# Optimization experiments

Measured on AMD Instinct MI355X. Metric: run time of the kernel, lower is better.

Reference implementation:

```python
import jax, jax.numpy as jnp
import numpy as np

B, N = 64, 4096          # trees per batch, leaves per complete binary tree
V, S = 21, 50            # amino-acid vocab, grammar-symbol vocab
E, H = 64, 128           # embed_dim, hidden_dim


def setup_inputs() -> dict:
    key = jax.random.key(0)
    ks = jax.random.split(key, 16)

    def lin_w(k, din, dout):
        return (jax.random.normal(k, (dout, din), jnp.float32) / np.sqrt(din)).astype(jnp.float32)

    tokens = jax.random.randint(ks[0], (B, N), 0, V, dtype=jnp.int32)
    symbols = jax.random.randint(ks[1], (B, N - 1), 0, S, dtype=jnp.int32)

    emb = jax.random.normal(ks[2], (V, E), jnp.float32) * 0.02
    emb = emb.at[0].set(0.0)  # padding_idx=0
    sym_emb = jax.random.normal(ks[3], (S, E), jnp.float32) * 0.02

    return {
        "tokens": tokens, "symbols": symbols,
        "emb": emb, "sym_emb": sym_emb,
        "Wp": lin_w(ks[4], E, H), "bp": jnp.zeros((H,), jnp.float32),
        "Wi": lin_w(ks[5], H, H), "bi": jnp.zeros((H,), jnp.float32),
        "Ui": lin_w(ks[6], H, H),
        "Wf": lin_w(ks[7], H, H), "bf": jnp.zeros((H,), jnp.float32),
        "Uf": lin_w(ks[8], H, H),
        "Wo": lin_w(ks[9], H, H), "bo": jnp.zeros((H,), jnp.float32),
        "Uo": lin_w(ks[10], H, H),
        "Wu": lin_w(ks[11], H, H), "bu": jnp.zeros((H,), jnp.float32),
        "Uu": lin_w(ks[12], H, H),
        "Wout": lin_w(ks[13], H, H), "bout": jnp.zeros((H,), jnp.float32),
    }


def _encode(tokens, symbols, emb, sym_emb, Wp, bp, Wi, bi, Ui, Wf, bf, Uf,
            Wo, bo, Uo, Wu, bu, Uu, Wout, bout):
    emb = emb.at[0].set(0.0)  # padding row contributes nothing (and gets no grad)

    # Leaf nodes: amino-acid embedding -> input_proj, no children.
    x = emb[tokens] @ Wp.T + bp                      # [B, N, H]
    i = jax.nn.sigmoid(x @ Wi.T + bi)
    o = jax.nn.sigmoid(x @ Wo.T + bo)
    u = jnp.tanh(x @ Wu.T + bu)
    c = i * u                                        # [B, N, H]
    h = o * jnp.tanh(c)

    # Bottom-up over levels of the complete binary tree (Child-Sum Tree-LSTM).
    off, n = 0, N
    while n > 1:
        m = n // 2
        xs = sym_emb[symbols[:, off:off + m]] @ Wp.T + bp   # [B, m, H]
        hl, hr = h[:, 0::2], h[:, 1::2]
        cl, cr = c[:, 0::2], c[:, 1::2]
        ht = hl + hr                                         # h_tilde = sum_j h_j
        gi = jax.nn.sigmoid(xs @ Wi.T + bi + ht @ Ui.T)
        go = jax.nn.sigmoid(xs @ Wo.T + bo + ht @ Uo.T)
        gu = jnp.tanh(xs @ Wu.T + bu + ht @ Uu.T)
        fx = xs @ Wf.T + bf
        fl = jax.nn.sigmoid(fx + hl @ Uf.T)                  # per-child forget gates
        fr = jax.nn.sigmoid(fx + hr @ Uf.T)
        c = gi * gu + fl * cl + fr * cr
        h = go * jnp.tanh(c)
        off += m
        n = m

    root_h = h[:, 0]                                         # [B, H]
    return root_h @ Wout.T + bout                            # output_proj


def reference(tokens, symbols, emb, sym_emb, Wp, bp, Wi, bi, Ui, Wf, bf, Uf,
              Wo, bo, Uo, Wu, bu, Uu, Wout, bout):
    return _encode(tokens, symbols, emb, sym_emb, Wp, bp, Wi, bi, Ui, Wf, bf,
                   Uf, Wo, bo, Uo, Wu, bu, Uu, Wout, bout)
```

## Files before the change

### kernel.cpp

```cpp
#include <hip/hip_runtime.h>
#include <hip/hip_bf16.h>

typedef __attribute__((ext_vector_type(8))) short short8;
typedef __attribute__((ext_vector_type(4))) float f32x4;

static constexpr int B_ = 64;
static constexpr int N_ = 4096;
static constexpr int V_ = 21;
static constexpr int S_ = 50;
static constexpr int E_ = 64;
static constexpr int H_ = 128;
static constexpr int NPAIR = V_ * V_;
static constexpr int NTAB = NPAIR * S_;

__device__ __forceinline__ float rcp_(float x) { return __builtin_amdgcn_rcpf(x); }
__device__ __forceinline__ float sigm(float x) { return rcp_(1.0f + __expf(-x)); }
__device__ __forceinline__ float tanh_(float x) {
  float a = fabsf(x);
  float e = __expf(-2.0f * a);
  float t = (1.0f - e) * rcp_(1.0f + e);
  return x < 0.0f ? -t : t;
}
__device__ __forceinline__ unsigned short f2bf(float f) {
  __hip_bfloat16 b = __float2bfloat16(f);
  return *reinterpret_cast<unsigned short*>(&b);
}
__device__ __forceinline__ float bf2f(unsigned short u) {
  return __uint_as_float(((unsigned int)u) << 16);
}

__global__ void k_pre(const float* __restrict__ emb, const float* __restrict__ sym_emb,
                      const float* __restrict__ Wp, const float* __restrict__ bp,
                      const float* __restrict__ Wi, const float* __restrict__ bi, const float* __restrict__ Ui,
                      const float* __restrict__ Wf, const float* __restrict__ bf, const float* __restrict__ Uf,
                      const float* __restrict__ Wo, const float* __restrict__ bo, const float* __restrict__ Uo,
                      const float* __restrict__ Wu, const float* __restrict__ bu, const float* __restrict__ Uu,
                      unsigned short* __restrict__ Wfrag, float* __restrict__ Wt,
                      unsigned short* __restrict__ leaf_h8, float* __restrict__ leaf_c,
                      float* __restrict__ symx) {
  int blk = blockIdx.x, t = threadIdx.x;
  if (blk < 32) {
    int idx = blk * 256 + t;
    int L = idx & 63;
    int K = (idx >> 6) & 3;
    int T = idx >> 8;
    int n = 16 * T + (L & 15);
    int k0 = 32 * K + ((L >> 4) << 3);
    int g = n >> 7, o = n & 127;
    const float* U = (g == 0) ? Ui : (g == 1) ? Uo : (g == 2) ? Uu : Uf;
    unsigned short out[8];
    #pragma unroll
    for (int j = 0; j < 8; ++j) out[j] = f2bf(U[o * 128 + k0 + j]);
    *(int4*)(Wfrag + (size_t)idx * 8) = *(int4*)out;
  } else if (blk < 32 + V_) {
    int v = blk - 32;
    __shared__ float x[128];
    if (t < 128) {
      float acc = bp[t];
      if (v != 0) {
        for (int e = 0; e < E_; ++e) acc = fmaf(emb[v * E_ + e], Wp[t * E_ + e], acc);
      }
      x[t] = acc;
    }
    __syncthreads();
    if (t < 128) {
      float zi = bi[t], zo = bo[t], zu = bu[t];
      for (int k = 0; k < H_; ++k) {
        float xv = x[k];
        zi = fmaf(xv, Wi[t * H_ + k], zi);
        zo = fmaf(xv, Wo[t * H_ + k], zo);
        zu = fmaf(xv, Wu[t * H_ + k], zu);
      }
      float gi = sigm(zi), go = sigm(zo), gu = tanh_(zu);
      float c = gi * gu;
      leaf_c[v * H_ + t] = c;
      leaf_h8[v * H_ + t] = f2bf(go * tanh_(c));
    }
  } else if (blk < 32 + V_ + S_) {
    int s = blk - 32 - V_;
    __shared__ float x[128];
    if (t < 128) {
      float acc = bp[t];
      for (int e = 0; e < E_; ++e) acc = fmaf(sym_emb[s * E_ + e], Wp[t * E_ + e], acc);
      x[t] = acc;
    }
    __syncthreads();
    if (t < 128) {
      float zi = bi[t], zo = bo[t], zu = bu[t], zf = bf[t];
      for (int k = 0; k < H_; ++k) {
        float xv = x[k];
        zi = fmaf(xv, Wi[t * H_ + k], zi);
        zo = fmaf(xv, Wo[t * H_ + k], zo);
        zu = fmaf(xv, Wu[t * H_ + k], zu);
        zf = fmaf(xv, Wf[t * H_ + k], zf);
      }
      size_t base = (size_t)s * 4 * H_;
      symx[base + 0 * H_ + t] = zi;
      symx[base + 1 * H_ + t] = zo;
      symx[base + 2 * H_ + t] = zu;
      symx[base + 3 * H_ + t] = zf;
    }
  } else {
    int base = ((blk - 103) * 256 + t) * 8;
    int k = base >> 9;
    int col = base & 511;
    int gg = col >> 7, o0 = col & 127;
    const float* U = (gg == 0) ? Ui : (gg == 1) ? Uo : (gg == 2) ? Uu : Uf;
    float v[8];
    #pragma unroll
    for (int j = 0; j < 8; ++j) v[j] = U[(o0 + j) * 128 + k];
    *(float4*)(Wt + base) = *(float4*)v;
    *(float4*)(Wt + base + 4) = *(float4*)(v + 4);
  }
}

__global__ void k_tabA(const unsigned short* __restrict__ leaf_h8, const float* __restrict__ Wt,
                       float* __restrict__ za) {
  int p = blockIdx.x, t = threadIdx.x;
  int tl = p / V_, tr = p % V_;
  __shared__ float hl[128], hr[128];
  hl[t] = bf2f(leaf_h8[tl * H_ + t]);
  hr[t] = bf2f(leaf_h8[tr * H_ + t]);
  __syncthreads();
  float zi = 0.f, zo = 0.f, zu = 0.f, pfl = 0.f, pfr = 0.f;
  for (int k = 0; k < H_; ++k) {
    float l = hl[k], r = hr[k], ht = l + r;
    const float* wr = Wt + k * 512;
    zi = fmaf(ht, wr[t], zi);
    zo = fmaf(ht, wr[128 + t], zo);
    zu = fmaf(ht, wr[256 + t], zu);
    float wf = wr[384 + t];
    pfl = fmaf(l, wf, pfl);
    pfr = fmaf(r, wf, pfr);
  }
  float* z = za + (size_t)p * 640;
  z[t] = zi; z[128 + t] = zo; z[256 + t] = zu; z[384 + t] = pfl; z[512 + t] = pfr;
}

__global__ void k_tabB(const float* __restrict__ za, const float* __restrict__ symx,
                       const float* __restrict__ leaf_c,
                       const int* __restrict__ tokens, const int* __restrict__ symbols,
                       unsigned short* __restrict__ tab_h8, float* __restrict__ tab_c,
                       int* __restrict__ idx1) {
  int blk = blockIdx.x, t = threadIdx.x;
  if (blk < NTAB / 2) {
    int row = blk * 2 + (t >> 7);
    int u = t & 127;
    int p = row / S_, s = row - p * S_;
    int tl = p / V_, tr = p - tl * V_;
    const float* z = za + (size_t)p * 640;
    const float* sx = symx + (size_t)s * 512;
    float gi = sigm(sx[u] + z[u]);
    float go = sigm(sx[128 + u] + z[128 + u]);
    float gu = tanh_(sx[256 + u] + z[256 + u]);
    float fx = sx[384 + u];
    float fl = sigm(fx + z[384 + u]);
    float fr = sigm(fx + z[512 + u]);
    float cv = fmaf(gi, gu, fmaf(fl, leaf_c[tl * H_ + u], fr * leaf_c[tr * H_ + u]));
    tab_c[(size_t)row * H_ + u] = cv;
    tab_h8[(size_t)row * H_ + u] = f2bf(go * tanh_(cv));
  } else {
    int g = (blk - NTAB / 2) * 256 + t;
    int b = g >> 11, j = g & 2047;
    idx1[g] = (tokens[b * N_ + 2 * j] * V_ + tokens[b * N_ + 2 * j + 1]) * S_ + symbols[b * (N_ - 1) + j];
  }
}

template <bool GATHER>
__global__ void __launch_bounds__(512, 2) k_level(
    const unsigned short* __restrict__ Wfrag, const float* __restrict__ symx,
    const int* __restrict__ symbols, int sym_off, int lgm,
    const unsigned short* __restrict__ h_prev8, const float* __restrict__ c_prev,
    const int* __restrict__ gidx,
    const unsigned short* __restrict__ gh8, const float* __restrict__ gc,
    unsigned short* __restrict__ h_out8, float* __restrict__ c_out) {
  __shared__ __align__(16) unsigned short Asm[32][136];
  int t = threadIdx.x;
  int w = t >> 6, L = t & 63, q = L >> 4, cL = L & 15;
  int g0 = blockIdx.x * 16;

  {
    int row = t >> 4, co = (t & 15) * 8;
    const unsigned short* src = GATHER
        ? gh8 + (size_t)gidx[2 * g0 + row] * H_ + co
        : h_prev8 + (size_t)(2 * g0 + row) * H_ + co;
    *(int4*)&Asm[row][co] = *(const int4*)src;
  }
  __syncthreads();

  f32x4 acc[2][4];
  #pragma unroll
  for (int r = 0; r < 2; ++r)
    #pragma unroll
    for (int g = 0; g < 4; ++g) acc[r][g] = (f32x4){0.f, 0.f, 0.f, 0.f};

  const short8* wf = (const short8*)Wfrag;
  #pragma unroll
  for (int K = 0; K < 4; ++K) {
    short8 bfr[4];
    #pragma unroll
    for (int g = 0; g < 4; ++g) bfr[g] = wf[(size_t)((w + 8 * g) * 4 + K) * 64 + L];
    short8 a0 = *(const short8*)&Asm[cL][K * 32 + q * 8];
    short8 a1 = *(const short8*)&Asm[16 + cL][K * 32 + q * 8];
    #pragma unroll
    for (int g = 0; g < 4; ++g) {
      acc[0][g] = __builtin_amdgcn_mfma_f32_16x16x32_bf16(a0, bfr[g], acc[0][g], 0, 0, 0);
      acc[1][g] = __builtin_amdgcn_mfma_f32_16x16x32_bf16(a1, bfr[g], acc[1][g], 0, 0, 0);
    }
  }

  int cc = 16 * w + cL;
  int mmask = (1 << lgm) - 1;
  #pragma unroll
  for (int r = 0; r < 2; ++r) {
    #pragma unroll
    for (int nd = 0; nd < 2; ++nd) {
      int n = 8 * r + 2 * q + nd;
      int g = g0 + n;
      int bb = g >> lgm, jj = g & mmask;
      int s = symbols[bb * (N_ - 1) + sym_off + jj];
      const float* sx = symx + (size_t)s * 512;
      const float* clp;
      const float* crp;
      if (GATHER) {
        clp = gc + (size_t)gidx[2 * g] * H_;
        crp = gc + (size_t)gidx[2 * g + 1] * H_;
      } else {
        clp = c_prev + (size_t)(2 * g) * H_;
        crp = c_prev + (size_t)(2 * g + 1) * H_;
      }
      float i_p = acc[r][0][2 * nd] + acc[r][0][2 * nd + 1];
      float o_p = acc[r][1][2 * nd] + acc[r][1][2 * nd + 1];
      float u_p = acc[r][2][2 * nd] + acc[r][2][2 * nd + 1];
      float fl_p = acc[r][3][2 * nd];
      float fr_p = acc[r][3][2 * nd + 1];
      float gi = sigm(sx[cc] + i_p);
      float go = sigm(sx[128 + cc] + o_p);
      float gu = tanh_(sx[256 + cc] + u_p);
      float fx = sx[384 + cc];
      float fl = sigm(fx + fl_p);
      float fr = sigm(fx + fr_p);
      float cv = fmaf(gi, gu, fmaf(fl, clp[cc], fr * crp[cc]));
      c_out[(size_t)g * H_ + cc] = cv;
      h_out8[(size_t)g * H_ + cc] = f2bf(go * tanh_(cv));
    }
  }
}

__global__ void __launch_bounds__(512, 1) k_deep(
    const unsigned short* __restrict__ Wfrag, const float* __restrict__ symx,
    const int* __restrict__ symbols,
    const unsigned short* __restrict__ in_h8, const float* __restrict__ in_c,
    float* __restrict__ out_root) {
  __shared__ __align__(16) unsigned short Asm[64][136];
  __shared__ float Csm0[64][128];
  __shared__ float Csm1[32][128];
  int t = threadIdx.x;
  int w = t >> 6, L = t & 63, q = L >> 4, cL = L & 15;
  int b = blockIdx.x;

  #pragma unroll
  for (int i = 0; i < 2; ++i) {
    int fid = t + 512 * i;
    int row = fid >> 4, co = (fid & 15) * 8;
    *(int4*)&Asm[row][co] = *(const int4*)(in_h8 + (size_t)(b * 64 + row) * H_ + co);
  }
  #pragma unroll
  for (int i = 0; i < 4; ++i) {
    int fid = t + 512 * i;
    int row = fid >> 5, c4 = (fid & 31) << 2;
    *(float4*)&Csm0[row][c4] = *(const float4*)(in_c + (size_t)(b * 64 + row) * H_ + c4);
  }
  __syncthreads();

  const short8* wf = (const short8*)Wfrag;
  int cc = 16 * w + cL;
  int R = 64;
  #pragma unroll
  for (int lev = 0; lev < 6; ++lev) {
    const int l = 7 + lev;
    const int nodes = R >> 1;
    const int jb = b * (N_ - 1) + (N_ - (N_ >> (l - 1)));
    const int nchunk = (R + 31) >> 5;
    for (int c = 0; c < nchunk; ++c) {
      f32x4 acc[2][4];
      #pragma unroll
      for (int r = 0; r < 2; ++r)
        #pragma unroll
        for (int g = 0; g < 4; ++g) acc[r][g] = (f32x4){0.f, 0.f, 0.f, 0.f};
      #pragma unroll
      for (int K = 0; K < 4; ++K) {
        short8 bfr[4];
        #pragma unroll
        for (int g = 0; g < 4; ++g) bfr[g] = wf[(size_t)((w + 8 * g) * 4 + K) * 64 + L];
        short8 a0 = *(const short8*)&Asm[32 * c + cL][K * 32 + q * 8];
        short8 a1 = *(const short8*)&Asm[32 * c + 16 + cL][K * 32 + q * 8];
        #pragma unroll
        for (int g = 0; g < 4; ++g) {
          acc[0][g] = __builtin_amdgcn_mfma_f32_16x16x32_bf16(a0, bfr[g], acc[0][g], 0, 0, 0);
          acc[1][g] = __builtin_amdgcn_mfma_f32_16x16x32_bf16(a1, bfr[g], acc[1][g], 0, 0, 0);
        }
      }
      __syncthreads();
      const float* crd = (l & 1) ? &Csm0[0][0] : &Csm1[0][0];
      float* cwr = (l & 1) ? &Csm1[0][0] : &Csm0[0][0];
      #pragma unroll
      for (int r = 0; r < 2; ++r) {
        #pragma unroll
        for (int nd = 0; nd < 2; ++nd) {
          int n = 16 * c + 8 * r + 2 * q + nd;
          if (n < nodes) {
            int s = symbols[jb + n];
            const float* sx = symx + (size_t)s * 512;
            float i_p = acc[r][0][2 * nd] + acc[r][0][2 * nd + 1];
            float o_p = acc[r][1][2 * nd] + acc[r][1][2 * nd + 1];
            float u_p = acc[r][2][2 * nd] + acc[r][2][2 * nd + 1];
            float fl_p = acc[r][3][2 * nd];
            float fr_p = acc[r][3][2 * nd + 1];
            float gi = sigm(sx[cc] + i_p);
            float go = sigm(sx[128 + cc] + o_p);
            float gu = tanh_(sx[256 + cc] + u_p);
            float fx = sx[384 + cc];
            float fl = sigm(fx + fl_p);
            float fr = sigm(fx + fr_p);
            float cv = fmaf(gi, gu, fmaf(fl, crd[(size_t)(2 * n) * 128 + cc],
                                         fr * crd[(size_t)(2 * n + 1) * 128 + cc]));
            float hv = go * tanh_(cv);
            if (lev == 5) {
              out_root[(size_t)b * H_ + cc] = hv;
            } else {
              cwr[(size_t)n * 128 + cc] = cv;
              Asm[n][cc] = f2bf(hv);
            }
          }
        }
      }
      __syncthreads();
    }
    R >>= 1;
  }
}

__global__ void k_out(const float* __restrict__ hroot, const float* __restrict__ Wout,
                      const float* __restrict__ bout, float* __restrict__ out) {
  int b = blockIdx.x, o = threadIdx.x;
  __shared__ float hr[128];
  hr[o] = hroot[(size_t)b * H_ + o];
  __syncthreads();
  float acc = bout[o];
  for (int k = 0; k < H_; ++k) acc = fmaf(hr[k], Wout[o * H_ + k], acc);
  out[(size_t)b * H_ + o] = acc;
}

extern "C" void kernel_launch(void* const* d_in, const int* in_sizes, int n_in,
                              void* d_out, int out_size, void* d_ws, size_t ws_size,
                              hipStream_t stream) {
  const int* tokens    = (const int*)d_in[0];
  const int* symbols   = (const int*)d_in[1];
  const float* emb     = (const float*)d_in[2];
  const float* sym_emb = (const float*)d_in[3];
  const float* Wp  = (const float*)d_in[4];
  const float* bp  = (const float*)d_in[5];
  const float* Wi  = (const float*)d_in[6];
  const float* bi  = (const float*)d_in[7];
  const float* Ui  = (const float*)d_in[8];
  const float* Wf  = (const float*)d_in[9];
  const float* bf  = (const float*)d_in[10];
  const float* Uf  = (const float*)d_in[11];
  const float* Wo  = (const float*)d_in[12];
  const float* bo  = (const float*)d_in[13];
  const float* Uo  = (const float*)d_in[14];
  const float* Wu  = (const float*)d_in[15];
  const float* bu  = (const float*)d_in[16];
  const float* Uu  = (const float*)d_in[17];
  const float* Wout= (const float*)d_in[18];
  const float* bout= (const float*)d_in[19];

  char* ws = (char*)d_ws;
  unsigned short* Wfrag   = (unsigned short*)(ws);
  float*          Wt      = (float*)(ws + 131072);
  unsigned short* leaf_h8 = (unsigned short*)(ws + 393216);
  float*          leaf_c  = (float*)(ws + 398592);
  float*          symx    = (float*)(ws + 409344);
  float*          za      = (float*)(ws + 511744);
  unsigned short* tab_h8  = (unsigned short*)(ws + 1640704);
  float*          tab_c   = (float*)(ws + 7285504UL);
  int*            idx1    = (int*)(ws + 18575104UL);
  float*          hroot   = (float*)(ws + 19099392UL);
  unsigned short* A_h8    = (unsigned short*)(ws + 19132160UL);
  float*          A_c     = (float*)(ws + 35909376UL);
  unsigned short* B_h8    = (unsigned short*)(ws + 69463808UL);
  float*          B_c     = (float*)(ws + 77852416UL);

  k_pre<<<135, 256, 0, stream>>>(emb, sym_emb, Wp, bp,
      Wi, bi, Ui, Wf, bf, Uf, Wo, bo, Uo, Wu, bu, Uu,
      Wfrag, Wt, leaf_h8, leaf_c, symx);
  k_tabA<<<NPAIR, 128, 0, stream>>>(leaf_h8, Wt, za);
  k_tabB<<<NTAB / 2 + 512, 256, 0, stream>>>(za, symx, leaf_c, tokens, symbols,
      tab_h8, tab_c, idx1);

  unsigned short* prev_h = nullptr;
  float* prev_c = nullptr;
  int off = 2048;
  for (int l = 2; l <= 6; ++l) {
    int m = N_ >> l;
    int M = B_ * m;
    int lgm = 12 - l;
    unsigned short* oh = (l & 1) ? B_h8 : A_h8;
    float* oc = (l & 1) ? B_c : A_c;
    if (l == 2) {
      k_level<true><<<M / 16, 512, 0, stream>>>(Wfrag, symx, symbols, off, lgm,
          nullptr, nullptr, idx1, tab_h8, tab_c, oh, oc);
    } else {
      k_level<false><<<M / 16, 512, 0, stream>>>(Wfrag, symx, symbols, off, lgm,
          prev_h, prev_c, nullptr, nullptr, nullptr, oh, oc);
    }
    prev_h = oh;
    prev_c = oc;
    off += m;
  }
  k_deep<<<B_, 512, 0, stream>>>(Wfrag, symx, symbols, prev_h, prev_c, hroot);
  k_out<<<B_, 128, 0, stream>>>(hroot, Wout, bout, (float*)d_out);
}
```

Baseline: 231.5 us.

## Fuse tree levels pairwise in LDS and parallelize precompute with transposed weights

Levels 2+3 and 4+5 of the bottom-up tree are now computed inside single kernels. The intermediate level's h and c stay in shared memory instead of going through global memory, which removes two kernel launches and the level-2 and level-4 global round trips. The precompute is split into a transpose kernel and an embedding kernel that reads transposed Wp/W matrices for coalesced access. The cost is more LDS per block and a smaller grid with less parallelism at the fused levels.

```diff
diff --git a/kernel.cpp b/kernel.cpp
--- a/kernel.cpp
+++ b/kernel.cpp
@@ -29,15 +29,27 @@
   return __uint_as_float(((unsigned int)u) << 16);
 }
 
-__global__ void k_pre(const float* __restrict__ emb, const float* __restrict__ sym_emb,
-                      const float* __restrict__ Wp, const float* __restrict__ bp,
-                      const float* __restrict__ Wi, const float* __restrict__ bi, const float* __restrict__ Ui,
-                      const float* __restrict__ Wf, const float* __restrict__ bf, const float* __restrict__ Uf,
-                      const float* __restrict__ Wo, const float* __restrict__ bo, const float* __restrict__ Uo,
-                      const float* __restrict__ Wu, const float* __restrict__ bu, const float* __restrict__ Uu,
-                      unsigned short* __restrict__ Wfrag, float* __restrict__ Wt,
-                      unsigned short* __restrict__ leaf_h8, float* __restrict__ leaf_c,
-                      float* __restrict__ symx) {
+struct Gates { float cv, hv; };
+__device__ __forceinline__ Gates gate_combine(const float* __restrict__ sx, int cc,
+    float i_p, float o_p, float u_p, float fl_p, float fr_p, float cl, float cr) {
+  float gi = sigm(sx[cc] + i_p);
+  float go = sigm(sx[128 + cc] + o_p);
+  float gu = tanh_(sx[256 + cc] + u_p);
+  float fx = sx[384 + cc];
+  float fl = sigm(fx + fl_p);
+  float fr = sigm(fx + fr_p);
+  float cv = fmaf(gi, gu, fmaf(fl, cl, fr * cr));
+  Gates g; g.cv = cv; g.hv = go * tanh_(cv);
+  return g;
+}
+
+__global__ void k_pre0(const float* __restrict__ Ui, const float* __restrict__ Uo,
+                       const float* __restrict__ Uu, const float* __restrict__ Uf,
+                       const float* __restrict__ Wi, const float* __restrict__ Wo,
+                       const float* __restrict__ Wu, const float* __restrict__ Wf,
+                       const float* __restrict__ Wp,
+                       unsigned short* __restrict__ Wfrag, float* __restrict__ Wt,
+                       float* __restrict__ Wxt, float* __restrict__ Wpt) {
   int blk = blockIdx.x, t = threadIdx.x;
   if (blk < 32) {
     int idx = blk * 256 + t;
@@ -52,65 +64,78 @@
     #pragma unroll
     for (int j = 0; j < 8; ++j) out[j] = f2bf(U[o * 128 + k0 + j]);
     *(int4*)(Wfrag + (size_t)idx * 8) = *(int4*)out;
-  } else if (blk < 32 + V_) {
-    int v = blk - 32;
-    __shared__ float x[128];
-    if (t < 128) {
-      float acc = bp[t];
-      if (v != 0) {
-        for (int e = 0; e < E_; ++e) acc = fmaf(emb[v * E_ + e], Wp[t * E_ + e], acc);
-      }
-      x[t] = acc;
-    }
-    __syncthreads();
-    if (t < 128) {
-      float zi = bi[t], zo = bo[t], zu = bu[t];
-      for (int k = 0; k < H_; ++k) {
-        float xv = x[k];
-        zi = fmaf(xv, Wi[t * H_ + k], zi);
-        zo = fmaf(xv, Wo[t * H_ + k], zo);
-        zu = fmaf(xv, Wu[t * H_ + k], zu);
-      }
-      float gi = sigm(zi), go = sigm(zo), gu = tanh_(zu);
-      float c = gi * gu;
-      leaf_c[v * H_ + t] = c;
-      leaf_h8[v * H_ + t] = f2bf(go * tanh_(c));
-    }
-  } else if (blk < 32 + V_ + S_) {
-    int s = blk - 32 - V_;
-    __shared__ float x[128];
-    if (t < 128) {
-      float acc = bp[t];
-      for (int e = 0; e < E_; ++e) acc = fmaf(sym_emb[s * E_ + e], Wp[t * E_ + e], acc);
-      x[t] = acc;
-    }
-    __syncthreads();
-    if (t < 128) {
-      float zi = bi[t], zo = bo[t], zu = bu[t], zf = bf[t];
-      for (int k = 0; k < H_; ++k) {
-        float xv = x[k];
-        zi = fmaf(xv, Wi[t * H_ + k], zi);
-        zo = fmaf(xv, Wo[t * H_ + k], zo);
-        zu = fmaf(xv, Wu[t * H_ + k], zu);
-        zf = fmaf(xv, Wf[t * H_ + k], zf);
-      }
-      size_t base = (size_t)s * 4 * H_;
-      symx[base + 0 * H_ + t] = zi;
-      symx[base + 1 * H_ + t] = zo;
-      symx[base + 2 * H_ + t] = zu;
-      symx[base + 3 * H_ + t] = zf;
-    }
-  } else {
-    int base = ((blk - 103) * 256 + t) * 8;
+  } else if (blk < 96) {
+    bool isU = blk < 64;
+    int base = (((blk & 31)) * 256 + t) * 8;
     int k = base >> 9;
     int col = base & 511;
     int gg = col >> 7, o0 = col & 127;
-    const float* U = (gg == 0) ? Ui : (gg == 1) ? Uo : (gg == 2) ? Uu : Uf;
+    const float* M;
+    if (isU) M = (gg == 0) ? Ui : (gg == 1) ? Uo : (gg == 2) ? Uu : Uf;
+    else     M = (gg == 0) ? Wi : (gg == 1) ? Wo : (gg == 2) ? Wu : Wf;
+    float* D = isU ? Wt : Wxt;
     float v[8];
     #pragma unroll
-    for (int j = 0; j < 8; ++j) v[j] = U[(o0 + j) * 128 + k];
-    *(float4*)(Wt + base) = *(float4*)v;
-    *(float4*)(Wt + base + 4) = *(float4*)(v + 4);
+    for (int j = 0; j < 8; ++j) v[j] = M[(o0 + j) * 128 + k];
+    *(float4*)(D + base) = *(float4*)v;
+    *(float4*)(D + base + 4) = *(float4*)(v + 4);
+  } else {
+    for (int i = t; i < E_ * H_; i += 256) {
+      int e = i >> 7, o = i & 127;
+      Wpt[i] = Wp[o * E_ + e];
+    }
+  }
+}
+
+__global__ void k_pre1(const float* __restrict__ emb, const float* __restrict__ sym_emb,
+                       const float* __restrict__ Wpt, const float* __restrict__ Wxt,
+                       const float* __restrict__ bp, const float* __restrict__ bi,
+                       const float* __restrict__ bo, const float* __restrict__ bu,
+                       const float* __restrict__ bfv,
+                       unsigned short* __restrict__ leaf_h8, float* __restrict__ leaf_c,
+                       float* __restrict__ symx) {
+  int blk = blockIdx.x, t = threadIdx.x;
+  __shared__ float x[128];
+  if (blk < V_) {
+    int v = blk;
+    float acc = bp[t];
+    if (v != 0) {
+      for (int e = 0; e < E_; ++e) acc = fmaf(emb[v * E_ + e], Wpt[e * 128 + t], acc);
+    }
+    x[t] = acc;
+    __syncthreads();
+    float zi = bi[t], zo = bo[t], zu = bu[t];
+    for (int k = 0; k < H_; ++k) {
+      float xv = x[k];
+      const float* wr = Wxt + k * 512;
+      zi = fmaf(xv, wr[t], zi);
+      zo = fmaf(xv, wr[128 + t], zo);
+      zu = fmaf(xv, wr[256 + t], zu);
+    }
+    float gi = sigm(zi), go = sigm(zo), gu = tanh_(zu);
+    float c = gi * gu;
+    leaf_c[v * H_ + t] = c;
+    leaf_h8[v * H_ + t] = f2bf(go * tanh_(c));
+  } else {
+    int s = blk - V_;
+    float acc = bp[t];
+    for (int e = 0; e < E_; ++e) acc = fmaf(sym_emb[s * E_ + e], Wpt[e * 128 + t], acc);
+    x[t] = acc;
+    __syncthreads();
+    float zi = bi[t], zo = bo[t], zu = bu[t], zf = bfv[t];
+    for (int k = 0; k < H_; ++k) {
+      float xv = x[k];
+      const float* wr = Wxt + k * 512;
+      zi = fmaf(xv, wr[t], zi);
+      zo = fmaf(xv, wr[128 + t], zo);
+      zu = fmaf(xv, wr[256 + t], zu);
+      zf = fmaf(xv, wr[384 + t], zf);
+    }
+    size_t base = (size_t)s * 4 * H_;
+    symx[base + 0 * H_ + t] = zi;
+    symx[base + 1 * H_ + t] = zo;
+    symx[base + 2 * H_ + t] = zu;
+    symx[base + 3 * H_ + t] = zf;
   }
 }
 
@@ -166,13 +191,221 @@
   }
 }
 
-template <bool GATHER>
-__global__ void __launch_bounds__(512, 2) k_level(
+__global__ void __launch_bounds__(512, 4) k_lvl23(
     const unsigned short* __restrict__ Wfrag, const float* __restrict__ symx,
-    const int* __restrict__ symbols, int sym_off, int lgm,
+    const int* __restrict__ symbols, const int* __restrict__ idx1,
+    const unsigned short* __restrict__ gh8, const float* __restrict__ gc,
+    unsigned short* __restrict__ h_out8, float* __restrict__ c_out) {
+  __shared__ __align__(16) unsigned short Ag[64][136];
+  __shared__ __align__(16) unsigned short Bh[32][136];
+  __shared__ float Bc[32][132];
+  int t = threadIdx.x;
+  int w = t >> 6, L = t & 63, q = L >> 4, cL = L & 15;
+  int cc = 16 * w + cL;
+  int g0 = blockIdx.x * 32;
+  int b = g0 >> 10;
+  int j2 = g0 & 1023;
+  const int* sym_b = symbols + (size_t)b * (N_ - 1);
+  const int* gix = idx1 + 2 * g0;
+
+  #pragma unroll
+  for (int i = 0; i < 2; ++i) {
+    int fid = t + 512 * i;
+    int row = fid >> 4, co = (fid & 15) * 8;
+    *(int4*)&Ag[row][co] = *(const int4*)(gh8 + (size_t)gix[row] * H_ + co);
+  }
+  __syncthreads();
+
+  const short8* wf = (const short8*)Wfrag;
+  #pragma unroll
+  for (int c = 0; c < 2; ++c) {
+    f32x4 acc[2][4];
+    #pragma unroll
+    for (int r = 0; r < 2; ++r)
+      #pragma unroll
+      for (int g = 0; g < 4; ++g) acc[r][g] = (f32x4){0.f, 0.f, 0.f, 0.f};
+    #pragma unroll
+    for (int K = 0; K < 4; ++K) {
+      short8 bfr[4];
+      #pragma unroll
+      for (int g = 0; g < 4; ++g) bfr[g] = wf[(size_t)((w + 8 * g) * 4 + K) * 64 + L];
+      short8 a0 = *(const short8*)&Ag[32 * c + cL][K * 32 + q * 8];
+      short8 a1 = *(const short8*)&Ag[32 * c + 16 + cL][K * 32 + q * 8];
+      #pragma unroll
+      for (int g = 0; g < 4; ++g) {
+        acc[0][g] = __builtin_amdgcn_mfma_f32_16x16x32_bf16(a0, bfr[g], acc[0][g], 0, 0, 0);
+        acc[1][g] = __builtin_amdgcn_mfma_f32_16x16x32_bf16(a1, bfr[g], acc[1][g], 0, 0, 0);
+      }
+    }
+    #pragma unroll
+    for (int r = 0; r < 2; ++r) {
+      #pragma unroll
+      for (int nd = 0; nd < 2; ++nd) {
+        int n = 16 * c + 8 * r + 2 * q + nd;
+        int s = sym_b[2048 + j2 + n];
+        const float* sx = symx + (size_t)s * 512;
+        float clv = gc[(size_t)gix[2 * n] * H_ + cc];
+        float crv = gc[(size_t)gix[2 * n + 1] * H_ + cc];
+        Gates gt = gate_combine(sx, cc,
+            acc[r][0][2 * nd] + acc[r][0][2 * nd + 1],
+            acc[r][1][2 * nd] + acc[r][1][2 * nd + 1],
+            acc[r][2][2 * nd] + acc[r][2][2 * nd + 1],
+            acc[r][3][2 * nd], acc[r][3][2 * nd + 1], clv, crv);
+        Bc[n][cc] = gt.cv;
+        Bh[n][cc] = f2bf(gt.hv);
+      }
+    }
+  }
+  __syncthreads();
+  {
+    f32x4 acc[2][4];
+    #pragma unroll
+    for (int r = 0; r < 2; ++r)
+      #pragma unroll
+      for (int g = 0; g < 4; ++g) acc[r][g] = (f32x4){0.f, 0.f, 0.f, 0.f};
+    #pragma unroll
+    for (int K = 0; K < 4; ++K) {
+      short8 bfr[4];
+      #pragma unroll
+      for (int g = 0; g < 4; ++g) bfr[g] = wf[(size_t)((w + 8 * g) * 4 + K) * 64 + L];
+      short8 a0 = *(const short8*)&Bh[cL][K * 32 + q * 8];
+      short8 a1 = *(const short8*)&Bh[16 + cL][K * 32 + q * 8];
+      #pragma unroll
+      for (int g = 0; g < 4; ++g) {
+        acc[0][g] = __builtin_amdgcn_mfma_f32_16x16x32_bf16(a0, bfr[g], acc[0][g], 0, 0, 0);
+        acc[1][g] = __builtin_amdgcn_mfma_f32_16x16x32_bf16(a1, bfr[g], acc[1][g], 0, 0, 0);
+      }
+    }
+    #pragma unroll
+    for (int r = 0; r < 2; ++r) {
+      #pragma unroll
+      for (int nd = 0; nd < 2; ++nd) {
+        int n = 8 * r + 2 * q + nd;
+        int G3 = (g0 >> 1) + n;
+        int s = sym_b[3072 + (j2 >> 1) + n];
+        const float* sx = symx + (size_t)s * 512;
+        Gates gt = gate_combine(sx, cc,
+            acc[r][0][2 * nd] + acc[r][0][2 * nd + 1],
+            acc[r][1][2 * nd] + acc[r][1][2 * nd + 1],
+            acc[r][2][2 * nd] + acc[r][2][2 * nd + 1],
+            acc[r][3][2 * nd], acc[r][3][2 * nd + 1],
+            Bc[2 * n][cc], Bc[2 * n + 1][cc]);
+        c_out[(size_t)G3 * H_ + cc] = gt.cv;
+        h_out8[(size_t)G3 * H_ + cc] = f2bf(gt.hv);
+      }
+    }
+  }
+}
+
+__global__ void __launch_bounds__(512, 4) k_lvl45(
+    const unsigned short* __restrict__ Wfrag, const float* __restrict__ symx,
+    const int* __restrict__ symbols,
+    const unsigned short* __restrict__ in_h8, const float* __restrict__ in_c,
+    unsigned short* __restrict__ h_out8, float* __restrict__ c_out) {
+  __shared__ __align__(16) unsigned short Ag[64][136];
+  __shared__ __align__(16) unsigned short Bh[32][136];
+  __shared__ float Bc[32][132];
+  int t = threadIdx.x;
+  int w = t >> 6, L = t & 63, q = L >> 4, cL = L & 15;
+  int cc = 16 * w + cL;
+  int g0 = blockIdx.x * 32;
+  int b = g0 >> 8;
+  int j4 = g0 & 255;
+  const int* sym_b = symbols + (size_t)b * (N_ - 1);
+
+  #pragma unroll
+  for (int i = 0; i < 2; ++i) {
+    int fid = t + 512 * i;
+    int row = fid >> 4, co = (fid & 15) * 8;
+    *(int4*)&Ag[row][co] = *(const int4*)(in_h8 + (size_t)(2 * g0 + row) * H_ + co);
+  }
+  __syncthreads();
+
+  const short8* wf = (const short8*)Wfrag;
+  #pragma unroll
+  for (int c = 0; c < 2; ++c) {
+    f32x4 acc[2][4];
+    #pragma unroll
+    for (int r = 0; r < 2; ++r)
+      #pragma unroll
+      for (int g = 0; g < 4; ++g) acc[r][g] = (f32x4){0.f, 0.f, 0.f, 0.f};
+    #pragma unroll
+    for (int K = 0; K < 4; ++K) {
+      short8 bfr[4];
+      #pragma unroll
+      for (int g = 0; g < 4; ++g) bfr[g] = wf[(size_t)((w + 8 * g) * 4 + K) * 64 + L];
+      short8 a0 = *(const short8*)&Ag[32 * c + cL][K * 32 + q * 8];
+      short8 a1 = *(const short8*)&Ag[32 * c + 16 + cL][K * 32 + q * 8];
+      #pragma unroll
+      for (int g = 0; g < 4; ++g) {
+        acc[0][g] = __builtin_amdgcn_mfma_f32_16x16x32_bf16(a0, bfr[g], acc[0][g], 0, 0, 0);
+        acc[1][g] = __builtin_amdgcn_mfma_f32_16x16x32_bf16(a1, bfr[g], acc[1][g], 0, 0, 0);
+      }
+    }
+    #pragma unroll
+    for (int r = 0; r < 2; ++r) {
+      #pragma unroll
+      for (int nd = 0; nd < 2; ++nd) {
+        int n = 16 * c + 8 * r + 2 * q + nd;
+        int g = g0 + n;
+        int s = sym_b[3584 + j4 + n];
+        const float* sx = symx + (size_t)s * 512;
+        Gates gt = gate_combine(sx, cc,
+            acc[r][0][2 * nd] + acc[r][0][2 * nd + 1],
+            acc[r][1][2 * nd] + acc[r][1][2 * nd + 1],
+            acc[r][2][2 * nd] + acc[r][2][2 * nd + 1],
+            acc[r][3][2 * nd], acc[r][3][2 * nd + 1],
+            in_c[(size_t)(2 * g) * H_ + cc], in_c[(size_t)(2 * g + 1) * H_ + cc]);
+        Bc[n][cc] = gt.cv;
+        Bh[n][cc] = f2bf(gt.hv);
+      }
+    }
+  }
+  __syncthreads();
+  {
+    f32x4 acc[2][4];
+    #pragma unroll
+    for (int r = 0; r < 2; ++r)
+      #pragma unroll
+      for (int g = 0; g < 4; ++g) acc[r][g] = (f32x4){0.f, 0.f, 0.f, 0.f};
+    #pragma unroll
+    for (int K = 0; K < 4; ++K) {
+      short8 bfr[4];
+      #pragma unroll
+      for (int g = 0; g < 4; ++g) bfr[g] = wf[(size_t)((w + 8 * g) * 4 + K) * 64 + L];
+      short8 a0 = *(const short8*)&Bh[cL][K * 32 + q * 8];
+      short8 a1 = *(const short8*)&Bh[16 + cL][K * 32 + q * 8];
+      #pragma unroll
+      for (int g = 0; g < 4; ++g) {
+        acc[0][g] = __builtin_amdgcn_mfma_f32_16x16x32_bf16(a0, bfr[g], acc[0][g], 0, 0, 0);
+        acc[1][g] = __builtin_amdgcn_mfma_f32_16x16x32_bf16(a1, bfr[g], acc[1][g], 0, 0, 0);
+      }
+    }
+    #pragma unroll
+    for (int r = 0; r < 2; ++r) {
+      #pragma unroll
+      for (int nd = 0; nd < 2; ++nd) {
+        int n = 8 * r + 2 * q + nd;
+        int G5 = (g0 >> 1) + n;
+        int s = sym_b[3840 + (j4 >> 1) + n];
+        const float* sx = symx + (size_t)s * 512;
+        Gates gt = gate_combine(sx, cc,
+            acc[r][0][2 * nd] + acc[r][0][2 * nd + 1],
+            acc[r][1][2 * nd] + acc[r][1][2 * nd + 1],
+            acc[r][2][2 * nd] + acc[r][2][2 * nd + 1],
+            acc[r][3][2 * nd], acc[r][3][2 * nd + 1],
+            Bc[2 * n][cc], Bc[2 * n + 1][cc]);
+        c_out[(size_t)G5 * H_ + cc] = gt.cv;
+        h_out8[(size_t)G5 * H_ + cc] = f2bf(gt.hv);
+      }
+    }
+  }
+}
+
+__global__ void __launch_bounds__(512, 2) k_lvl6(
+    const unsigned short* __restrict__ Wfrag, const float* __restrict__ symx,
+    const int* __restrict__ symbols,
     const unsigned short* __restrict__ h_prev8, const float* __restrict__ c_prev,
-    const int* __restrict__ gidx,
-    const unsigned short* __restrict__ gh8, const float* __restrict__ gc,
     unsigned short* __restrict__ h_out8, float* __restrict__ c_out) {
   __shared__ __align__(16) unsigned short Asm[32][136];
   int t = threadIdx.x;
@@ -181,10 +414,7 @@
 
   {
     int row = t >> 4, co = (t & 15) * 8;
-    const unsigned short* src = GATHER
-        ? gh8 + (size_t)gidx[2 * g0 + row] * H_ + co
-        : h_prev8 + (size_t)(2 * g0 + row) * H_ + co;
-    *(int4*)&Asm[row][co] = *(const int4*)src;
+    *(int4*)&Asm[row][co] = *(const int4*)(h_prev8 + (size_t)(2 * g0 + row) * H_ + co);
   }
   __syncthreads();
 
@@ -210,39 +440,23 @@
   }
 
   int cc = 16 * w + cL;
-  int mmask = (1 << lgm) - 1;
   #pragma unroll
   for (int r = 0; r < 2; ++r) {
     #pragma unroll
     for (int nd = 0; nd < 2; ++nd) {
       int n = 8 * r + 2 * q + nd;
       int g = g0 + n;
-      int bb = g >> lgm, jj = g & mmask;
-      int s = symbols[bb * (N_ - 1) + sym_off + jj];
+      int bb = g >> 6, jj = g & 63;
+      int s = symbols[bb * (N_ - 1) + 3968 + jj];
       const float* sx = symx + (size_t)s * 512;
-      const float* clp;
-      const float* crp;
-      if (GATHER) {
-        clp = gc + (size_t)gidx[2 * g] * H_;
-        crp = gc + (size_t)gidx[2 * g + 1] * H_;
-      } else {
-        clp = c_prev + (size_t)(2 * g) * H_;
-        crp = c_prev + (size_t)(2 * g + 1) * H_;
-      }
-      float i_p = acc[r][0][2 * nd] + acc[r][0][2 * nd + 1];
-      float o_p = acc[r][1][2 * nd] + acc[r][1][2 * nd + 1];
-      float u_p = acc[r][2][2 * nd] + acc[r][2][2 * nd + 1];
-      float fl_p = acc[r][3][2 * nd];
-      float fr_p = acc[r][3][2 * nd + 1];
-      float gi = sigm(sx[cc] + i_p);
-      float go = sigm(sx[128 + cc] + o_p);
-      float gu = tanh_(sx[256 + cc] + u_p);
-      float fx = sx[384 + cc];
-      float fl = sigm(fx + fl_p);
-      float fr = sigm(fx + fr_p);
-      float cv = fmaf(gi, gu, fmaf(fl, clp[cc], fr * crp[cc]));
-      c_out[(size_t)g * H_ + cc] = cv;
-      h_out8[(size_t)g * H_ + cc] = f2bf(go * tanh_(cv));
+      Gates gt = gate_combine(sx, cc,
+          acc[r][0][2 * nd] + acc[r][0][2 * nd + 1],
+          acc[r][1][2 * nd] + acc[r][1][2 * nd + 1],
+          acc[r][2][2 * nd] + acc[r][2][2 * nd + 1],
+          acc[r][3][2 * nd], acc[r][3][2 * nd + 1],
+          c_prev[(size_t)(2 * g) * H_ + cc], c_prev[(size_t)(2 * g + 1) * H_ + cc]);
+      c_out[(size_t)g * H_ + cc] = gt.cv;
+      h_out8[(size_t)g * H_ + cc] = f2bf(gt.hv);
     }
   }
 }
@@ -312,25 +526,17 @@
           if (n < nodes) {
             int s = symbols[jb + n];
             const float* sx = symx + (size_t)s * 512;
-            float i_p = acc[r][0][2 * nd] + acc[r][0][2 * nd + 1];
-            float o_p = acc[r][1][2 * nd] + acc[r][1][2 * nd + 1];
-            float u_p = acc[r][2][2 * nd] + acc[r][2][2 * nd + 1];
-            float fl_p = acc[r][3][2 * nd];
-            float fr_p = acc[r][3][2 * nd + 1];
-            float gi = sigm(sx[cc] + i_p);
-            float go = sigm(sx[128 + cc] + o_p);
-            float gu = tanh_(sx[256 + cc] + u_p);
-            float fx = sx[384 + cc];
-            float fl = sigm(fx + fl_p);
-            float fr = sigm(fx + fr_p);
-            float cv = fmaf(gi, gu, fmaf(fl, crd[(size_t)(2 * n) * 128 + cc],
-                                         fr * crd[(size_t)(2 * n + 1) * 128 + cc]));
-            float hv = go * tanh_(cv);
+            Gates gt = gate_combine(sx, cc,
+                acc[r][0][2 * nd] + acc[r][0][2 * nd + 1],
+                acc[r][1][2 * nd] + acc[r][1][2 * nd + 1],
+                acc[r][2][2 * nd] + acc[r][2][2 * nd + 1],
+                acc[r][3][2 * nd], acc[r][3][2 * nd + 1],
+                crd[(size_t)(2 * n) * 128 + cc], crd[(size_t)(2 * n + 1) * 128 + cc]);
             if (lev == 5) {
-              out_root[(size_t)b * H_ + cc] = hv;
+              out_root[(size_t)b * H_ + cc] = gt.hv;
             } else {
-              cwr[(size_t)n * 128 + cc] = cv;
-              Asm[n][cc] = f2bf(hv);
+              cwr[(size_t)n * 128 + cc] = gt.cv;
+              Asm[n][cc] = f2bf(gt.hv);
             }
           }
         }
@@ -379,46 +585,33 @@
   char* ws = (char*)d_ws;
   unsigned short* Wfrag   = (unsigned short*)(ws);
   float*          Wt      = (float*)(ws + 131072);
-  unsigned short* leaf_h8 = (unsigned short*)(ws + 393216);
-  float*          leaf_c  = (float*)(ws + 398592);
-  float*          symx    = (float*)(ws + 409344);
-  float*          za      = (float*)(ws + 511744);
-  unsigned short* tab_h8  = (unsigned short*)(ws + 1640704);
-  float*          tab_c   = (float*)(ws + 7285504UL);
-  int*            idx1    = (int*)(ws + 18575104UL);
-  float*          hroot   = (float*)(ws + 19099392UL);
-  unsigned short* A_h8    = (unsigned short*)(ws + 19132160UL);
-  float*          A_c     = (float*)(ws + 35909376UL);
-  unsigned short* B_h8    = (unsigned short*)(ws + 69463808UL);
-  float*          B_c     = (float*)(ws + 77852416UL);
-
-  k_pre<<<135, 256, 0, stream>>>(emb, sym_emb, Wp, bp,
-      Wi, bi, Ui, Wf, bf, Uf, Wo, bo, Uo, Wu, bu, Uu,
-      Wfrag, Wt, leaf_h8, leaf_c, symx);
+  float*          Wxt     = (float*)(ws + 393216);
+  float*          Wpt     = (float*)(ws + 655360);
+  unsigned short* leaf_h8 = (unsigned short*)(ws + 688128);
+  float*          leaf_c  = (float*)(ws + 693504);
+  float*          symx    = (float*)(ws + 704256);
+  float*          za      = (float*)(ws + 806656);
+  unsigned short* tab_h8  = (unsigned short*)(ws + 1935616);
+  float*          tab_c   = (float*)(ws + 7580416UL);
+  int*            idx1    = (int*)(ws + 18870016UL);
+  float*          hroot   = (float*)(ws + 19394304UL);
+  unsigned short* L3h8    = (unsigned short*)(ws + 19427072UL);
+  float*          L3c     = (float*)(ws + 27815680UL);
+  unsigned short* L5h8    = (unsigned short*)(ws + 44592896UL);
+  float*          L5c     = (float*)(ws + 46690048UL);
+  unsigned short* L6h8    = (unsigned short*)(ws + 50884352UL);
+  float*          L6c     = (float*)(ws + 51932928UL);
+
+  k_pre0<<<97, 256, 0, stream>>>(Ui, Uo, Uu, Uf, Wi, Wo, Wu, Wf, Wp,
+                                 Wfrag, Wt, Wxt, Wpt);
+  k_pre1<<<V_ + S_, 128, 0, stream>>>(emb, sym_emb, Wpt, Wxt,
+                                      bp, bi, bo, bu, bf, leaf_h8, leaf_c, symx);
   k_tabA<<<NPAIR, 128, 0, stream>>>(leaf_h8, Wt, za);
   k_tabB<<<NTAB / 2 + 512, 256, 0, stream>>>(za, symx, leaf_c, tokens, symbols,
-      tab_h8, tab_c, idx1);
-
-  unsigned short* prev_h = nullptr;
-  float* prev_c = nullptr;
-  int off = 2048;
-  for (int l = 2; l <= 6; ++l) {
-    int m = N_ >> l;
-    int M = B_ * m;
-    int lgm = 12 - l;
-    unsigned short* oh = (l & 1) ? B_h8 : A_h8;
-    float* oc = (l & 1) ? B_c : A_c;
-    if (l == 2) {
-      k_level<true><<<M / 16, 512, 0, stream>>>(Wfrag, symx, symbols, off, lgm,
-          nullptr, nullptr, idx1, tab_h8, tab_c, oh, oc);
-    } else {
-      k_level<false><<<M / 16, 512, 0, stream>>>(Wfrag, symx, symbols, off, lgm,
-          prev_h, prev_c, nullptr, nullptr, nullptr, oh, oc);
-    }
-    prev_h = oh;
-    prev_c = oc;
-    off += m;
-  }
-  k_deep<<<B_, 512, 0, stream>>>(Wfrag, symx, symbols, prev_h, prev_c, hroot);
+                                             tab_h8, tab_c, idx1);
+  k_lvl23<<<2048, 512, 0, stream>>>(Wfrag, symx, symbols, idx1, tab_h8, tab_c, L3h8, L3c);
+  k_lvl45<<<512, 512, 0, stream>>>(Wfrag, symx, symbols, L3h8, L3c, L5h8, L5c);
+  k_lvl6<<<256, 512, 0, stream>>>(Wfrag, symx, symbols, L5h8, L5c, L6h8, L6c);
+  k_deep<<<B_, 512, 0, stream>>>(Wfrag, symx, symbols, L6h8, L6c, hroot);
   k_out<<<B_, 128, 0, stream>>>(hroot, Wout, bout, (float*)d_out);
 }
```

Result: slower. 236.7 us (+2.2%).
